# Performance work log

Measured on AMD Instinct MI355X. Metric: run time of the kernel, lower is better.

## Reference

```python
import jax, jax.numpy as jnp
import numpy as np

HEAD = 128
BLOCK = 16
MAX_POS = 32768


def _rope_cache(dim=HEAD, base=10000.0, max_pos=MAX_POS):
    # Mirrors PrecomputedRotaryEmbedding: inv_freq/t in bf16, then cos/sin.
    inv = (1.0 / base ** (jnp.arange(0, dim, 2, dtype=jnp.float32) / dim)).astype(jnp.bfloat16)
    t = jnp.arange(max_pos, dtype=jnp.bfloat16)
    freqs = t[:, None] * inv[None, :]                      # [P, dim/2]
    emb = jnp.concatenate([freqs, freqs], axis=-1)         # [P, dim]
    return jnp.cos(emb).astype(jnp.float32), jnp.sin(emb).astype(jnp.float32)


def _rotary(x, cos, sin):
    # x: [B, H, D], cos/sin: [B, D]
    d2 = x.shape[-1] // 2
    rot = jnp.concatenate([-x[..., d2:], x[..., :d2]], axis=-1)
    return x * cos[:, None, :] + rot * sin[:, None, :]


def setup_inputs() -> dict:
    key = jax.random.key(0)
    ks = jax.random.split(key, 8)
    B, H, Hkv, D = 32, 32, 8, 128
    blocks_per_seq, bs = 128, BLOCK
    nblk = B * blocks_per_seq
    query = jax.random.normal(ks[0], (B, H, D), dtype=jnp.float32)
    k_new = jax.random.normal(ks[1], (B, Hkv, D), dtype=jnp.float32)
    v_new = jax.random.normal(ks[2], (B, Hkv, D), dtype=jnp.float32)
    k_cache = jax.random.normal(ks[3], (nblk, bs, Hkv, D), dtype=jnp.float32)
    v_cache = jax.random.normal(ks[4], (nblk, bs, Hkv, D), dtype=jnp.float32)
    block_table = jnp.arange(nblk, dtype=jnp.int32).reshape(B, blocks_per_seq)
    context_lens = jax.random.randint(ks[5], (B,), 1, 2048, dtype=jnp.int32)
    return {"query": query, "key": k_new, "value": v_new,
            "k_cache": k_cache, "v_cache": v_cache,
            "block_table": block_table, "context_lens": context_lens}


def reference(query, key, value, k_cache, v_cache, block_table, context_lens):
    B, H, D = query.shape
    Hkv = key.shape[1]
    nblk, bs, _, _ = k_cache.shape
    max_ctx = block_table.shape[1] * bs

    cos_c, sin_c = _rope_cache(dim=D)
    pos = context_lens.astype(jnp.int32)
    cos, sin = cos_c[pos], sin_c[pos]                      # [B, D]
    q = _rotary(query, cos, sin)                           # [B, H, D]
    k_new = _rotary(key, cos, sin)                         # [B, Hkv, D]

    # Scatter new k/v into the paged cache at slot of token (ctx - 1).
    last = pos - 1
    slot = block_table[jnp.arange(B), last // bs] * bs + last % bs  # [B]
    kf = k_cache.reshape(nblk * bs, Hkv, D).at[slot].set(k_new)
    vf = v_cache.reshape(nblk * bs, Hkv, D).at[slot].set(value)

    # Gather per-sequence KV via block table (irregular paged access).
    t = jnp.arange(max_ctx)
    idx = block_table[:, t // bs].astype(jnp.int32) * bs + (t % bs)[None, :].astype(jnp.int32)  # [B, L]
    idx = jnp.clip(idx, 0, nblk * bs - 1)
    K = kf[idx]                                            # [B, L, Hkv, D]
    V = vf[idx]

    scale = D ** -0.5
    g = H // Hkv
    qg = q.reshape(B, Hkv, g, D)
    scores = jnp.einsum('bkgd,blkd->bkgl', qg, K) * scale  # [B, Hkv, g, L]
    valid = t[None, :] < pos[:, None]                      # [B, L]
    scores = jnp.where(valid[:, None, None, :], scores, -1e30)
    p = jax.nn.softmax(scores, axis=-1)
    out = jnp.einsum('bkgl,blkd->bkgd', p, V)              # [B, Hkv, g, D]
    return out.reshape(B, H, D)
```

## Files before the change

kernel.cpp:

```cpp
#include <hip/hip_runtime.h>
#include <hip/hip_bf16.h>
#include <math.h>

#define NB 32
#define NH 32
#define HKV 8
#define GQ 4
#define DH 128
#define BS 16
#define BPS 128
#define MAXC 2048
#define NSPLIT 32
#define HSTR 132
#define PART_STRIDE (GQ * HSTR)

__device__ __forceinline__ float bf16r(float x) {
    return __bfloat162float(__float2bfloat16(x));
}

__global__ void prep_kernel(const float* __restrict__ q,
                            const float* __restrict__ knew,
                            const int* __restrict__ bt,
                            const int* __restrict__ ctx,
                            float* __restrict__ q_rot,
                            float* __restrict__ k_rot,
                            int* __restrict__ rowidx)
{
    __shared__ int slot_l[NB];
    int tid = threadIdx.x, bid = blockIdx.x;
    if (tid < NB) {
        int last = ctx[tid] - 1;
        slot_l[tid] = bt[tid * BPS + (last >> 4)] * BS + (last & 15);
    }
    __syncthreads();

    int g = bid * 256 + tid;
    int b = g >> 11;
    int t = g & (MAXC - 1);
    int flat = bt[b * BPS + (t >> 4)] * BS + (t & 15);
    int o = flat;
    #pragma unroll
    for (int j = 0; j < NB; ++j)
        if (flat == slot_l[j]) o = -(j + 1);
    rowidx[g] = o;

    if (bid < NB) {
        int rb  = bid;
        int d   = tid & 127;
        int hi  = tid >> 7;
        int pos = ctx[rb];
        int i2  = d & 63;
        float e   = (float)i2 * (1.0f / 64.0f);
        float pf  = (float)pow(10000.0, (double)e);
        float inv = bf16r(1.0f / pf);
        float tb  = bf16r((float)pos);
        float fr  = bf16r(tb * inv);
        float c   = bf16r(cosf(fr));
        float s   = bf16r(sinf(fr));

        const float* qb = q + (size_t)rb * NH * DH;
        float* qo = q_rot + (size_t)rb * NH * DH;
        #pragma unroll 4
        for (int h = hi * 16; h < hi * 16 + 16; ++h) {
            float x  = qb[h * DH + d];
            float xr = (d < 64) ? -qb[h * DH + d + 64] : qb[h * DH + d - 64];
            qo[h * DH + d] = x * c + xr * s;
        }
        const float* kb = knew + (size_t)rb * HKV * DH;
        float* ko = k_rot + (size_t)rb * HKV * DH;
        #pragma unroll
        for (int h = hi * 4; h < hi * 4 + 4; ++h) {
            float x  = kb[h * DH + d];
            float xr = (d < 64) ? -kb[h * DH + d + 64] : kb[h * DH + d - 64];
            ko[h * DH + d] = x * c + xr * s;
        }
    }
}

__global__ __launch_bounds__(256) void attn_partial(
    const float* __restrict__ kc, const float* __restrict__ vc,
    const float* __restrict__ vnew,
    const int* __restrict__ ctx,
    const float* __restrict__ q_rot, const float* __restrict__ k_rot,
    const int* __restrict__ rowidx, float* __restrict__ part)
{
    int tid = threadIdx.x;
    int bid = blockIdx.x;
    int w   = tid >> 6;
    int b   = bid & (NB - 1);
    int kvh = ((bid >> 5) & 1) * 4 + w;
    int sp  = bid >> 6;

    int L = ctx[b];
    int chunk = (L + NSPLIT - 1) / NSPLIT;
    int start = sp * chunk;
    int end   = min(L, start + chunk);

    int lane = tid & 63;
    int c    = lane & 31;
    int H    = lane >> 5;

    float4 qr[4];
    #pragma unroll
    for (int h = 0; h < 4; ++h)
        qr[h] = *(const float4*)(q_rot + ((size_t)b * NH + kvh * GQ + h) * DH + c * 4);

    float  m[4], l[4];
    float4 o[4];
    #pragma unroll
    for (int h = 0; h < 4; ++h) {
        m[h] = -INFINITY; l[h] = 0.f;
        o[h] = make_float4(0.f, 0.f, 0.f, 0.f);
    }

    const float scale = 0.08838834764831845f;

    for (int t0 = start; t0 < end; t0 += 8) {
        int src[4];
        #pragma unroll
        for (int i = 0; i < 4; ++i) {
            int t = min(t0 + 2 * i + H, end - 1);
            src[i] = rowidx[(b << 11) | t];
        }
        float4 kr[4], vr[4];
        #pragma unroll
        for (int i = 0; i < 4; ++i) {
            int oi = src[i]; int j = -oi - 1;
            const float* kp = (oi >= 0)
                ? kc + (size_t)oi * (HKV * DH) + kvh * DH
                : k_rot + ((size_t)j * HKV + kvh) * DH;
            kr[i] = ((const float4*)kp)[c];
        }
        #pragma unroll
        for (int i = 0; i < 4; ++i) {
            int oi = src[i]; int j = -oi - 1;
            const float* vp = (oi >= 0)
                ? vc + (size_t)oi * (HKV * DH) + kvh * DH
                : vnew + ((size_t)j * HKV + kvh) * DH;
            vr[i] = ((const float4*)vp)[c];
        }

        float s[4][4];
        #pragma unroll
        for (int i = 0; i < 4; ++i)
            #pragma unroll
            for (int h = 0; h < 4; ++h)
                s[i][h] = qr[h].x * kr[i].x + qr[h].y * kr[i].y
                        + qr[h].z * kr[i].z + qr[h].w * kr[i].w;

        #pragma unroll
        for (int lev = 1; lev <= 16; lev <<= 1)
            #pragma unroll
            for (int i = 0; i < 4; ++i)
                #pragma unroll
                for (int h = 0; h < 4; ++h)
                    s[i][h] += __shfl_xor(s[i][h], lev);

        #pragma unroll
        for (int i = 0; i < 4; ++i) {
            bool valid = (t0 + 2 * i + H) < end;
            #pragma unroll
            for (int h = 0; h < 4; ++h)
                s[i][h] = valid ? s[i][h] * scale : -INFINITY;
        }

        #pragma unroll
        for (int h = 0; h < 4; ++h) {
            float tm = fmaxf(fmaxf(s[0][h], s[1][h]), fmaxf(s[2][h], s[3][h]));
            float mnew = fmaxf(m[h], tm);
            if (mnew > -INFINITY) {
                float r  = __expf(m[h] - mnew);
                float p0 = __expf(s[0][h] - mnew);
                float p1 = __expf(s[1][h] - mnew);
                float p2 = __expf(s[2][h] - mnew);
                float p3 = __expf(s[3][h] - mnew);
                l[h] = l[h] * r + (p0 + p1 + p2 + p3);
                o[h].x = o[h].x * r + p0 * vr[0].x + p1 * vr[1].x + p2 * vr[2].x + p3 * vr[3].x;
                o[h].y = o[h].y * r + p0 * vr[0].y + p1 * vr[1].y + p2 * vr[2].y + p3 * vr[3].y;
                o[h].z = o[h].z * r + p0 * vr[0].z + p1 * vr[1].z + p2 * vr[2].z + p3 * vr[3].z;
                o[h].w = o[h].w * r + p0 * vr[0].w + p1 * vr[1].w + p2 * vr[2].w + p3 * vr[3].w;
                m[h] = mnew;
            }
        }
    }

    float* pw = part + (size_t)((b * HKV + kvh) * NSPLIT + sp) * PART_STRIDE;
    #pragma unroll
    for (int h = 0; h < 4; ++h) {
        float mo = __shfl_xor(m[h], 32);
        float M  = fmaxf(m[h], mo);
        float f  = (m[h] > -INFINITY) ? __expf(m[h] - M) : 0.f;
        float lf = l[h] * f;
        float lt = lf + __shfl_xor(lf, 32);
        float ox = o[h].x * f, oy = o[h].y * f, oz = o[h].z * f, ow = o[h].w * f;
        ox += __shfl_xor(ox, 32);
        oy += __shfl_xor(oy, 32);
        oz += __shfl_xor(oz, 32);
        ow += __shfl_xor(ow, 32);
        float* pp = pw + h * HSTR;
        if (H == 0) {
            pp[c * 4 + 0] = ox; pp[c * 4 + 1] = oy;
            pp[c * 4 + 2] = oz; pp[c * 4 + 3] = ow;
        }
        if (lane == 0) { pp[128] = M; pp[129] = lt; }
    }
}

__global__ void reduce_kernel(const float* __restrict__ part,
                              float* __restrict__ out)
{
    int blk = blockIdx.x;
    int d   = threadIdx.x;
    int b   = blk >> 5;
    int hq  = blk & 31;
    int kvh = hq >> 2;
    int g   = hq & 3;
    const float* base = part + (size_t)((b * HKV + kvh) * NSPLIT) * PART_STRIDE + g * HSTR;

    float M = -INFINITY;
    #pragma unroll 8
    for (int s = 0; s < NSPLIT; ++s)
        M = fmaxf(M, base[(size_t)s * PART_STRIDE + 128]);
    float S = 0.f, acc = 0.f;
    #pragma unroll 8
    for (int s = 0; s < NSPLIT; ++s) {
        float ms = base[(size_t)s * PART_STRIDE + 128];
        float f  = __expf(ms - M);
        S   += base[(size_t)s * PART_STRIDE + 129] * f;
        acc += base[(size_t)s * PART_STRIDE + d] * f;
    }
    out[(size_t)blk * DH + d] = acc / S;
}

extern "C" void kernel_launch(void* const* d_in, const int* in_sizes, int n_in,
                              void* d_out, int out_size, void* d_ws, size_t ws_size,
                              hipStream_t stream)
{
    const float* q    = (const float*)d_in[0];
    const float* knew = (const float*)d_in[1];
    const float* vnew = (const float*)d_in[2];
    const float* kc   = (const float*)d_in[3];
    const float* vc   = (const float*)d_in[4];
    const int*   bt   = (const int*)d_in[5];
    const int*   ctx  = (const int*)d_in[6];
    float* out = (float*)d_out;

    float* ws     = (float*)d_ws;
    float* q_rot  = ws;
    float* k_rot  = ws + 131072;
    int*   rowidx = (int*)(ws + 131072 + 32768);
    float* part   = ws + 131072 + 32768 + 65536;

    prep_kernel<<<NB * MAXC / 256, 256, 0, stream>>>(q, knew, bt, ctx,
                                                     q_rot, k_rot, rowidx);
    attn_partial<<<NB * 2 * NSPLIT, 256, 0, stream>>>(
        kc, vc, vnew, ctx, q_rot, k_rot, rowidx, part);
    reduce_kernel<<<NB * NH, 128, 0, stream>>>(part, out);
}
```

Baseline: 81.77 us.

## Map all KV heads of a token to one block and drop cross-half merge

Each attention block now covers all eight KV heads for one (sequence, split) pair. Each half-wave owns one KV head, so the block reads whole contiguous cache rows per token instead of different heads split across blocks. Both half-waves walk the same tokens, which removes the shuffle-based merge of two online-softmax states at the end and the guard against an all-masked max. A `__syncthreads` every eight tiles keeps the waves in step so they share cache lines. The grid is halved, which reduces the number of waves available to hide latency and adds barrier overhead.

Measured after the change: 82.40 us. About the same (+0.8%).

```diff
diff --git a/kernel.cpp b/kernel.cpp
--- a/kernel.cpp
+++ b/kernel.cpp
@@ -84,22 +84,21 @@
     const float* __restrict__ q_rot, const float* __restrict__ k_rot,
     const int* __restrict__ rowidx, float* __restrict__ part)
 {
-    int tid = threadIdx.x;
-    int bid = blockIdx.x;
-    int w   = tid >> 6;
-    int b   = bid & (NB - 1);
-    int kvh = ((bid >> 5) & 1) * 4 + w;
-    int sp  = bid >> 6;
+    int tid  = threadIdx.x;
+    int bid  = blockIdx.x;
+    int b    = bid & (NB - 1);
+    int sp   = bid >> 5;
+    int w    = tid >> 6;
+    int lane = tid & 63;
+    int c    = lane & 31;
+    int H    = lane >> 5;
+    int kvh  = 2 * w + H;
 
     int L = ctx[b];
     int chunk = (L + NSPLIT - 1) / NSPLIT;
     int start = sp * chunk;
     int end   = min(L, start + chunk);
 
-    int lane = tid & 63;
-    int c    = lane & 31;
-    int H    = lane >> 5;
-
     float4 qr[4];
     #pragma unroll
     for (int h = 0; h < 4; ++h)
@@ -114,30 +113,23 @@
     }
 
     const float scale = 0.08838834764831845f;
-
-    for (int t0 = start; t0 < end; t0 += 8) {
-        int src[4];
+    int tiles = 0;
+
+    for (int t0 = start; t0 < end; t0 += 4) {
+        float4 kr[4], vr[4];
         #pragma unroll
         for (int i = 0; i < 4; ++i) {
-            int t = min(t0 + 2 * i + H, end - 1);
-            src[i] = rowidx[(b << 11) | t];
-        }
-        float4 kr[4], vr[4];
-        #pragma unroll
-        for (int i = 0; i < 4; ++i) {
-            int oi = src[i]; int j = -oi - 1;
+            int t  = min(t0 + i, end - 1);
+            int oi = rowidx[(b << 11) | t];
+            int j  = -oi - 1;
             const float* kp = (oi >= 0)
-                ? kc + (size_t)oi * (HKV * DH) + kvh * DH
-                : k_rot + ((size_t)j * HKV + kvh) * DH;
-            kr[i] = ((const float4*)kp)[c];
-        }
-        #pragma unroll
-        for (int i = 0; i < 4; ++i) {
-            int oi = src[i]; int j = -oi - 1;
+                ? kc + (size_t)oi * (HKV * DH)
+                : k_rot + (size_t)j * (HKV * DH);
             const float* vp = (oi >= 0)
-                ? vc + (size_t)oi * (HKV * DH) + kvh * DH
-                : vnew + ((size_t)j * HKV + kvh) * DH;
-            vr[i] = ((const float4*)vp)[c];
+                ? vc + (size_t)oi * (HKV * DH)
+                : vnew + (size_t)j * (HKV * DH);
+            kr[i] = ((const float4*)(kp + kvh * DH))[c];
+            vr[i] = ((const float4*)(vp + kvh * DH))[c];
         }
 
         float s[4][4];
@@ -158,7 +150,7 @@
 
         #pragma unroll
         for (int i = 0; i < 4; ++i) {
-            bool valid = (t0 + 2 * i + H) < end;
+            bool valid = (t0 + i) < end;
             #pragma unroll
             for (int h = 0; h < 4; ++h)
                 s[i][h] = valid ? s[i][h] * scale : -INFINITY;
@@ -168,41 +160,28 @@
         for (int h = 0; h < 4; ++h) {
             float tm = fmaxf(fmaxf(s[0][h], s[1][h]), fmaxf(s[2][h], s[3][h]));
             float mnew = fmaxf(m[h], tm);
-            if (mnew > -INFINITY) {
-                float r  = __expf(m[h] - mnew);
-                float p0 = __expf(s[0][h] - mnew);
-                float p1 = __expf(s[1][h] - mnew);
-                float p2 = __expf(s[2][h] - mnew);
-                float p3 = __expf(s[3][h] - mnew);
-                l[h] = l[h] * r + (p0 + p1 + p2 + p3);
-                o[h].x = o[h].x * r + p0 * vr[0].x + p1 * vr[1].x + p2 * vr[2].x + p3 * vr[3].x;
-                o[h].y = o[h].y * r + p0 * vr[0].y + p1 * vr[1].y + p2 * vr[2].y + p3 * vr[3].y;
-                o[h].z = o[h].z * r + p0 * vr[0].z + p1 * vr[1].z + p2 * vr[2].z + p3 * vr[3].z;
-                o[h].w = o[h].w * r + p0 * vr[0].w + p1 * vr[1].w + p2 * vr[2].w + p3 * vr[3].w;
-                m[h] = mnew;
-            }
-        }
+            float r  = __expf(m[h] - mnew);
+            float p0 = __expf(s[0][h] - mnew);
+            float p1 = __expf(s[1][h] - mnew);
+            float p2 = __expf(s[2][h] - mnew);
+            float p3 = __expf(s[3][h] - mnew);
+            l[h] = l[h] * r + (p0 + p1 + p2 + p3);
+            o[h].x = o[h].x * r + p0 * vr[0].x + p1 * vr[1].x + p2 * vr[2].x + p3 * vr[3].x;
+            o[h].y = o[h].y * r + p0 * vr[0].y + p1 * vr[1].y + p2 * vr[2].y + p3 * vr[3].y;
+            o[h].z = o[h].z * r + p0 * vr[0].z + p1 * vr[1].z + p2 * vr[2].z + p3 * vr[3].z;
+            o[h].w = o[h].w * r + p0 * vr[0].w + p1 * vr[1].w + p2 * vr[2].w + p3 * vr[3].w;
+            m[h] = mnew;
+        }
+
+        if ((++tiles & 7) == 0) __syncthreads();
     }
 
     float* pw = part + (size_t)((b * HKV + kvh) * NSPLIT + sp) * PART_STRIDE;
     #pragma unroll
     for (int h = 0; h < 4; ++h) {
-        float mo = __shfl_xor(m[h], 32);
-        float M  = fmaxf(m[h], mo);
-        float f  = (m[h] > -INFINITY) ? __expf(m[h] - M) : 0.f;
-        float lf = l[h] * f;
-        float lt = lf + __shfl_xor(lf, 32);
-        float ox = o[h].x * f, oy = o[h].y * f, oz = o[h].z * f, ow = o[h].w * f;
-        ox += __shfl_xor(ox, 32);
-        oy += __shfl_xor(oy, 32);
-        oz += __shfl_xor(oz, 32);
-        ow += __shfl_xor(ow, 32);
         float* pp = pw + h * HSTR;
-        if (H == 0) {
-            pp[c * 4 + 0] = ox; pp[c * 4 + 1] = oy;
-            pp[c * 4 + 2] = oz; pp[c * 4 + 3] = ow;
-        }
-        if (lane == 0) { pp[128] = M; pp[129] = lt; }
+        *(float4*)&pp[c * 4] = o[h];
+        if (c == 0) { pp[128] = m[h]; pp[129] = l[h]; }
     }
 }
 
@@ -253,7 +232,7 @@
 
     prep_kernel<<<NB * MAXC / 256, 256, 0, stream>>>(q, knew, bt, ctx,
                                                      q_rot, k_rot, rowidx);
-    attn_partial<<<NB * 2 * NSPLIT, 256, 0, stream>>>(
+    attn_partial<<<NB * NSPLIT, 256, 0, stream>>>(
         kc, vc, vnew, ctx, q_rot, k_rot, rowidx, part);
     reduce_kernel<<<NB * NH, 128, 0, stream>>>(part, out);
 }
```
